# Performance work log

Hardware: AMD Instinct MI355X
Metric: run time of the kernel (lower is better)

The kernel has to match this reference:

```python
import jax, jax.numpy as jnp
import numpy as np

# physics constants (from initBatteryParams)
R_GAS = 8.3144621
F = 96487.0
ALPHA = 0.5
VOL = 2.2e-5
VOLS = 0.1 * VOL
VOLB = VOL - VOLS
SN = 2e-4
SP = 2e-4
KN = 2e4
KP = 2e4
TO = 10.0
TSN = 90.0
TSP = 90.0
U0P = 4.03
U0N = 0.01
QMAX_BASE = 10000.0
RO_BASE = 10.0
DT = 1.0

B = 2097152


def setup_inputs() -> dict:
    key = jax.random.key(0)
    ks = jax.random.split(key, 10)
    f32 = jnp.float32
    # per-batch learned params (qMax ~ 14000/10000, Ro ~ 0.15/10)
    qMax = jnp.full((B,), 1.4, dtype=f32)
    Ro = jnp.full((B,), 0.015, dtype=f32)
    tDiffusion = jnp.asarray(7e6, dtype=f32)
    # physically plausible initial state (get_initial_state): Tb=292.1, V's ~0,
    # qnB~qnBMax=7560, qnS~qnSMax=840, qpB~qpBMin=5040, qpS~qpSMin=560
    n = lambda k, s: jax.random.normal(k, s, dtype=f32)
    Tb = jnp.full((B,), 292.1, dtype=f32)
    Vo = 0.01 * n(ks[0], (B,))
    Vsn = 0.01 * n(ks[1], (B,))
    Vsp = 0.01 * n(ks[2], (B,))
    qnB = 7560.0 * (1.0 + 0.01 * n(ks[3], (B,)))
    qnS = 840.0 * (1.0 + 0.01 * n(ks[4], (B,)))
    qpB = 5040.0 * (1.0 + 0.01 * n(ks[5], (B,)))
    qpS = 560.0 * (1.0 + 0.01 * n(ks[6], (B,)))
    states = jnp.stack([Tb, Vo, Vsn, Vsp, qnB, qnS, qpB, qpS], axis=1)
    # applied current ~ [1, 3) A
    inputs = 1.0 + 2.0 * jax.random.uniform(ks[7], (B, 1), dtype=f32)
    # MLPp: Dense(1->8 tanh) -> Dense(8->4 tanh) -> Dense(4->1); MLPn: Dense(1->1)
    wk = jax.random.split(ks[8], 4)
    Wp1 = 0.5 * n(wk[0], (1, 8)); bp1 = jnp.zeros((8,), f32)
    Wp2 = 0.5 * n(wk[1], (8, 4)); bp2 = jnp.zeros((4,), f32)
    Wp3 = 0.5 * n(wk[2], (4, 1)); bp3 = jnp.zeros((1,), f32)
    Wn = jnp.full((1, 1), 0.0016, dtype=f32)  # MLPn fit to map [0,1]->[-8e-4,8e-4]
    bn = jnp.full((1,), -0.0008, dtype=f32)
    return dict(inputs=inputs, states=states, qMax=qMax, Ro=Ro,
                tDiffusion=tDiffusion, Wp1=Wp1, bp1=bp1, Wp2=Wp2, bp2=bp2,
                Wp3=Wp3, bp3=bp3, Wn=Wn, bn=bn)


def _battery_step(inputs, states, qMax, Ro, tDiffusion,
                  Wp1, bp1, Wp2, bp2, Wp3, bp3, Wn, bn):
    Tb, Vo, Vsn, Vsp, qnB, qnS, qpB, qpS = [states[:, k] for k in range(8)]
    i = inputs[:, 0]
    qSMax = qMax * QMAX_BASE * VOLS / VOL  # [B]

    # ---- getNextState ----
    xpS = jnp.clip(qpS / qSMax, 1e-18, 1.0)
    xnS = jnp.clip(qnS / qSMax, 1e-18, 1.0)
    Jn0 = 1e-18 + KN * (1.0 - xnS) ** ALPHA * xnS ** ALPHA
    Jp0 = 1e-18 + KP * (1.0 - xpS) ** ALPHA * xpS ** ALPHA
    qdotDiffBSn = (qnB / VOLB - qnS / VOLS) / tDiffusion
    qdotDiffBSp = (qpB / VOLB - qpS / VOLS) / tDiffusion
    Vodot = (i * Ro * RO_BASE - Vo) / TO
    VsnNom = R_GAS * Tb / F / ALPHA * jnp.arcsinh((i / SN) / (2.0 * Jn0))
    VspNom = R_GAS * Tb / F / ALPHA * jnp.arcsinh((i / SP) / (2.0 * Jp0))
    Vsndot = (VsnNom - Vsn) / TSN
    Vspdot = (VspNom - Vsp) / TSP
    Xnew = jnp.stack([
        Tb,                               # Tbdot = 0
        Vo + Vodot * DT,
        Vsn + Vsndot * DT,
        Vsp + Vspdot * DT,
        qnB - qdotDiffBSn * DT,
        qnS + (qdotDiffBSn - i) * DT,
        qpB - qdotDiffBSp * DT,
        qpS + (i + qdotDiffBSp) * DT,
    ], axis=1)  # [B,8]

    # ---- getNextOutput (on Xnew) ----
    Tb2, Vo2, Vsn2, Vsp2 = Xnew[:, 0], Xnew[:, 1], Xnew[:, 2], Xnew[:, 3]
    xpS2 = Xnew[:, 7] / qSMax  # no clip here, matching original
    xnS2 = Xnew[:, 5] / qSMax
    h = jnp.tanh(xpS2[:, None] @ Wp1 + bp1)
    h = jnp.tanh(h @ Wp2 + bp2)
    VepMLP = (h @ Wp3 + bp3)[:, 0]
    VenMLP = (xnS2[:, None] @ Wn + bn)[:, 0]
    safe_log_p = jnp.clip((1.0 - xpS2) / xpS2, 1e-18, 1e18)
    safe_log_n = jnp.clip((1.0 - xnS2) / xnS2, 1e-18, 1e18)
    Vep = U0P + R_GAS * Tb2 / F * jnp.log(safe_log_p) + VepMLP
    Ven = U0N + R_GAS * Tb2 / F * jnp.log(safe_log_n) + VenMLP
    V = Vep - Ven - Vo2 - Vsn2 - Vsp2
    return V[:, None], Xnew


def reference(inputs, states, qMax, Ro, tDiffusion,
              Wp1, bp1, Wp2, bp2, Wp3, bp3, Wn, bn):
    return _battery_step(inputs, states, qMax, Ro, tDiffusion,
                         Wp1, bp1, Wp2, bp2, Wp3, bp3, Wn, bn)
```

## Files before the change

kernel.cpp:

```cpp
#include <hip/hip_runtime.h>

#define DEVFN __device__ __forceinline__

DEVFN float fast_rcp(float x) { return __builtin_amdgcn_rcpf(x); }

DEVFN float fast_tanh(float x) {
    float e = __expf(2.0f * x);
    return 1.0f - 2.0f * fast_rcp(e + 1.0f);
}

DEVFN float fast_asinh(float z) {
    float az = fabsf(z);
    float r = __logf(az + sqrtf(fmaf(az, az, 1.0f)));
    return copysignf(r, z);
}

constexpr int ELEMS = 4;

DEVFN void battery_compute(
    float4 s0, float4 s1, float i, float qm, float ro, float invTD,
    const float* __restrict__ Wp1, const float* __restrict__ bp1,
    const float* __restrict__ Wp2, const float* __restrict__ bp2,
    const float* __restrict__ Wp3, const float* __restrict__ bp3,
    const float* __restrict__ Wn,  const float* __restrict__ bn,
    float& V, float4& o0, float4& o1)
{
    const float invVOLB = 1.0f / 1.98e-5f;
    const float invVOLS = 1.0f / 2.2e-6f;
    const float RTFA    = 8.3144621f / 96487.0f / 0.5f;
    const float RF      = 8.3144621f / 96487.0f;

    const float Tb = s0.x, Vo = s0.y, Vsn = s0.z, Vsp = s0.w;
    const float qnB = s1.x, qnS = s1.y, qpB = s1.z, qpS = s1.w;

    const float qSMax = qm * 1000.0f;
    const float rq    = fast_rcp(qSMax);

    float xpS = fminf(fmaxf(qpS * rq, 1e-18f), 1.0f);
    float xnS = fminf(fmaxf(qnS * rq, 1e-18f), 1.0f);

    float Jn0 = 1e-18f + 20000.0f * sqrtf((1.0f - xnS) * xnS);
    float Jp0 = 1e-18f + 20000.0f * sqrtf((1.0f - xpS) * xpS);

    float qdotn = (qnB * invVOLB - qnS * invVOLS) * invTD;
    float qdotp = (qpB * invVOLB - qpS * invVOLS) * invTD;

    float Vodot = (i * ro * 10.0f - Vo) * 0.1f;

    float zn = i * 2500.0f * fast_rcp(Jn0);
    float zp = i * 2500.0f * fast_rcp(Jp0);
    float VsnNom = RTFA * Tb * fast_asinh(zn);
    float VspNom = RTFA * Tb * fast_asinh(zp);

    const float X0 = Tb;
    const float X1 = Vo + Vodot;
    const float X2 = Vsn + (VsnNom - Vsn) * (1.0f / 90.0f);
    const float X3 = Vsp + (VspNom - Vsp) * (1.0f / 90.0f);
    const float X4 = qnB - qdotn;
    const float X5 = qnS + (qdotn - i);
    const float X6 = qpB - qdotp;
    const float X7 = qpS + (i + qdotp);

    const float xp2 = X7 * rq;
    const float xn2 = X5 * rq;

    float h1[8];
#pragma unroll
    for (int j = 0; j < 8; ++j)
        h1[j] = fast_tanh(fmaf(xp2, Wp1[j], bp1[j]));

    float h2[4];
#pragma unroll
    for (int k = 0; k < 4; ++k) {
        float acc = bp2[k];
#pragma unroll
        for (int j = 0; j < 8; ++j)
            acc = fmaf(h1[j], Wp2[j * 4 + k], acc);
        h2[k] = fast_tanh(acc);
    }

    float VepMLP = bp3[0];
#pragma unroll
    for (int k = 0; k < 4; ++k)
        VepMLP = fmaf(h2[k], Wp3[k], VepMLP);

    const float VenMLP = fmaf(xn2, Wn[0], bn[0]);

    float ratio = ((1.0f - xp2) * xn2) * fast_rcp(xp2 * (1.0f - xn2));
    float logr  = __logf(ratio);

    V = (4.03f - 0.01f) + RF * X0 * logr + VepMLP - VenMLP - X1 - X2 - X3;
    o0 = make_float4(X0, X1, X2, X3);
    o1 = make_float4(X4, X5, X6, X7);
}

template<bool EXACT>
__global__ __launch_bounds__(256) void battery_step_kernel(
    const float* __restrict__ inputs, const float* __restrict__ states,
    const float* __restrict__ qMax, const float* __restrict__ Ro,
    const float* __restrict__ tDiff,
    const float* __restrict__ Wp1, const float* __restrict__ bp1,
    const float* __restrict__ Wp2, const float* __restrict__ bp2,
    const float* __restrict__ Wp3, const float* __restrict__ bp3,
    const float* __restrict__ Wn,  const float* __restrict__ bn,
    float* __restrict__ outV, float* __restrict__ outX, int n)
{
    const int t      = blockIdx.x * 256 + threadIdx.x;
    const int stride = gridDim.x * 256;

    const float invTD = fast_rcp(tDiff[0]);

    int idx = t;
    float4 s0, s1; float cur, qm, ro;
    bool ok = EXACT || (idx < n);
    if (ok) {
        s0  = ((const float4*)states)[idx * 2 + 0];
        s1  = ((const float4*)states)[idx * 2 + 1];
        cur = inputs[idx];
        qm  = qMax[idx];
        ro  = Ro[idx];
    }

#pragma unroll
    for (int e = 0; e < ELEMS; ++e) {
        float4 ns0, ns1; float ncur, nqm, nro;
        bool nok = false;
        if (e + 1 < ELEMS) {
            int nidx = idx + stride;
            nok = EXACT || (nidx < n);
            if (nok) {
                ns0  = ((const float4*)states)[nidx * 2 + 0];
                ns1  = ((const float4*)states)[nidx * 2 + 1];
                ncur = inputs[nidx];
                nqm  = qMax[nidx];
                nro  = Ro[nidx];
            }
        }

        if (ok) {
            float V; float4 o0, o1;
            battery_compute(s0, s1, cur, qm, ro, invTD,
                            Wp1, bp1, Wp2, bp2, Wp3, bp3, Wn, bn,
                            V, o0, o1);
            outV[idx] = V;
            ((float4*)outX)[idx * 2 + 0] = o0;
            ((float4*)outX)[idx * 2 + 1] = o1;
        }

        idx += stride;
        s0 = ns0; s1 = ns1; cur = ncur; qm = nqm; ro = nro; ok = nok;
    }
}

__global__ __launch_bounds__(256) void stream_probe_kernel(
    const float* __restrict__ inputs, const float* __restrict__ states,
    const float* __restrict__ qMax, const float* __restrict__ Ro,
    float* __restrict__ wsOut)
{
    const int t      = blockIdx.x * 256 + threadIdx.x;
    const int stride = gridDim.x * 256;
    float acc = 0.0f;
#pragma unroll
    for (int e = 0; e < ELEMS; ++e) {
        int idx = t + e * stride;
        float4 s0 = ((const float4*)states)[idx * 2 + 0];
        float4 s1 = ((const float4*)states)[idx * 2 + 1];
        acc += s0.x + s0.y + s0.z + s0.w + s1.x + s1.y + s1.z + s1.w
             + inputs[idx] + qMax[idx] + Ro[idx];
        wsOut[idx] = acc;
    }
}

extern "C" void kernel_launch(void* const* d_in, const int* in_sizes, int n_in,
                              void* d_out, int out_size, void* d_ws, size_t ws_size,
                              hipStream_t stream) {
    const float* inputs = (const float*)d_in[0];
    const float* states = (const float*)d_in[1];
    const float* qMax   = (const float*)d_in[2];
    const float* Ro     = (const float*)d_in[3];
    const float* tDiff  = (const float*)d_in[4];
    const float* Wp1    = (const float*)d_in[5];
    const float* bp1    = (const float*)d_in[6];
    const float* Wp2    = (const float*)d_in[7];
    const float* bp2    = (const float*)d_in[8];
    const float* Wp3    = (const float*)d_in[9];
    const float* bp3    = (const float*)d_in[10];
    const float* Wn     = (const float*)d_in[11];
    const float* bn     = (const float*)d_in[12];

    const int n = in_sizes[0];
    float* outV = (float*)d_out;
    float* outX = (float*)d_out + n;

    const int threads = 256;
    const int chunk   = threads * ELEMS;

    if (n % chunk == 0) {
        const int blocks = n / chunk;
        battery_step_kernel<true><<<dim3(blocks), dim3(threads), 0, stream>>>(
            inputs, states, qMax, Ro, tDiff,
            Wp1, bp1, Wp2, bp2, Wp3, bp3, Wn, bn, outV, outX, n);
        if (ws_size >= (size_t)n * sizeof(float)) {
            stream_probe_kernel<<<dim3(blocks), dim3(threads), 0, stream>>>(
                inputs, states, qMax, Ro, (float*)d_ws);
        }
    } else {
        const int blocks = (n + chunk - 1) / chunk;
        battery_step_kernel<false><<<dim3(blocks), dim3(threads), 0, stream>>>(
            inputs, states, qMax, Ro, tDiff,
            Wp1, bp1, Wp2, bp2, Wp3, bp3, Wn, bn, outV, outX, n);
    }
}
```

Baseline: 188.4 us.

## Drop probe kernel, batch all loads upfront, use rsqrt and nontemporal stores

Removes the extra streaming probe kernel that re-read the inputs after the main step kernel, eliminating a redundant memory pass. The main kernel now processes 8 elements per thread and issues all loads before computing, and writes outputs with nontemporal stores. The Jn0/Jp0 reciprocal-of-sqrt path is replaced by a single rsqrt with the tiny additive epsilon dropped, and launch bounds request 4 waves of occupancy. Holding more loaded data in registers may raise register pressure.

```diff
diff --git a/kernel.cpp b/kernel.cpp
--- a/kernel.cpp
+++ b/kernel.cpp
@@ -2,7 +2,10 @@
 
 #define DEVFN __device__ __forceinline__
 
-DEVFN float fast_rcp(float x) { return __builtin_amdgcn_rcpf(x); }
+typedef float f32x4 __attribute__((ext_vector_type(4)));
+
+DEVFN float fast_rcp(float x)   { return __builtin_amdgcn_rcpf(x); }
+DEVFN float fast_rsqrt(float x) { return __builtin_amdgcn_rsqf(x); }
 
 DEVFN float fast_tanh(float x) {
     float e = __expf(2.0f * x);
@@ -15,15 +18,15 @@
     return copysignf(r, z);
 }
 
-constexpr int ELEMS = 4;
+constexpr int ELEMS = 8;
 
 DEVFN void battery_compute(
-    float4 s0, float4 s1, float i, float qm, float ro, float invTD,
+    f32x4 s0, f32x4 s1, float i, float qm, float ro, float invTD,
     const float* __restrict__ Wp1, const float* __restrict__ bp1,
     const float* __restrict__ Wp2, const float* __restrict__ bp2,
     const float* __restrict__ Wp3, const float* __restrict__ bp3,
     const float* __restrict__ Wn,  const float* __restrict__ bn,
-    float& V, float4& o0, float4& o1)
+    float& V, f32x4& o0, f32x4& o1)
 {
     const float invVOLB = 1.0f / 1.98e-5f;
     const float invVOLS = 1.0f / 2.2e-6f;
@@ -39,16 +42,16 @@
     float xpS = fminf(fmaxf(qpS * rq, 1e-18f), 1.0f);
     float xnS = fminf(fmaxf(qnS * rq, 1e-18f), 1.0f);
 
-    float Jn0 = 1e-18f + 20000.0f * sqrtf((1.0f - xnS) * xnS);
-    float Jp0 = 1e-18f + 20000.0f * sqrtf((1.0f - xpS) * xpS);
+    float un = (1.0f - xnS) * xnS;
+    float up = (1.0f - xpS) * xpS;
+    float zn = i * 0.125f * fast_rsqrt(fmaxf(un, 1e-30f));
+    float zp = i * 0.125f * fast_rsqrt(fmaxf(up, 1e-30f));
 
     float qdotn = (qnB * invVOLB - qnS * invVOLS) * invTD;
     float qdotp = (qpB * invVOLB - qpS * invVOLS) * invTD;
 
     float Vodot = (i * ro * 10.0f - Vo) * 0.1f;
 
-    float zn = i * 2500.0f * fast_rcp(Jn0);
-    float zp = i * 2500.0f * fast_rcp(Jp0);
     float VsnNom = RTFA * Tb * fast_asinh(zn);
     float VspNom = RTFA * Tb * fast_asinh(zp);
 
@@ -90,12 +93,12 @@
     float logr  = __logf(ratio);
 
     V = (4.03f - 0.01f) + RF * X0 * logr + VepMLP - VenMLP - X1 - X2 - X3;
-    o0 = make_float4(X0, X1, X2, X3);
-    o1 = make_float4(X4, X5, X6, X7);
+    o0.x = X0; o0.y = X1; o0.z = X2; o0.w = X3;
+    o1.x = X4; o1.y = X5; o1.z = X6; o1.w = X7;
 }
 
 template<bool EXACT>
-__global__ __launch_bounds__(256) void battery_step_kernel(
+__global__ __launch_bounds__(256, 4) void battery_step_kernel(
     const float* __restrict__ inputs, const float* __restrict__ states,
     const float* __restrict__ qMax, const float* __restrict__ Ro,
     const float* __restrict__ tDiff,
@@ -110,64 +113,33 @@
 
     const float invTD = fast_rcp(tDiff[0]);
 
-    int idx = t;
-    float4 s0, s1; float cur, qm, ro;
-    bool ok = EXACT || (idx < n);
-    if (ok) {
-        s0  = ((const float4*)states)[idx * 2 + 0];
-        s1  = ((const float4*)states)[idx * 2 + 1];
-        cur = inputs[idx];
-        qm  = qMax[idx];
-        ro  = Ro[idx];
+    f32x4 s0[ELEMS], s1[ELEMS];
+    float cur[ELEMS], qm[ELEMS], ro[ELEMS];
+    bool  ok[ELEMS];
+#pragma unroll
+    for (int e = 0; e < ELEMS; ++e) {
+        const int idx = t + e * stride;
+        ok[e] = EXACT || (idx < n);
+        if (ok[e]) {
+            s0[e]  = ((const f32x4*)states)[idx * 2 + 0];
+            s1[e]  = ((const f32x4*)states)[idx * 2 + 1];
+            cur[e] = inputs[idx];
+            qm[e]  = qMax[idx];
+            ro[e]  = Ro[idx];
+        }
     }
 
 #pragma unroll
     for (int e = 0; e < ELEMS; ++e) {
-        float4 ns0, ns1; float ncur, nqm, nro;
-        bool nok = false;
-        if (e + 1 < ELEMS) {
-            int nidx = idx + stride;
-            nok = EXACT || (nidx < n);
-            if (nok) {
-                ns0  = ((const float4*)states)[nidx * 2 + 0];
-                ns1  = ((const float4*)states)[nidx * 2 + 1];
-                ncur = inputs[nidx];
-                nqm  = qMax[nidx];
-                nro  = Ro[nidx];
-            }
-        }
-
-        if (ok) {
-            float V; float4 o0, o1;
-            battery_compute(s0, s1, cur, qm, ro, invTD,
-                            Wp1, bp1, Wp2, bp2, Wp3, bp3, Wn, bn,
-                            V, o0, o1);
-            outV[idx] = V;
-            ((float4*)outX)[idx * 2 + 0] = o0;
-            ((float4*)outX)[idx * 2 + 1] = o1;
-        }
-
-        idx += stride;
-        s0 = ns0; s1 = ns1; cur = ncur; qm = nqm; ro = nro; ok = nok;
-    }
-}
-
-__global__ __launch_bounds__(256) void stream_probe_kernel(
-    const float* __restrict__ inputs, const float* __restrict__ states,
-    const float* __restrict__ qMax, const float* __restrict__ Ro,
-    float* __restrict__ wsOut)
-{
-    const int t      = blockIdx.x * 256 + threadIdx.x;
-    const int stride = gridDim.x * 256;
-    float acc = 0.0f;
-#pragma unroll
-    for (int e = 0; e < ELEMS; ++e) {
-        int idx = t + e * stride;
-        float4 s0 = ((const float4*)states)[idx * 2 + 0];
-        float4 s1 = ((const float4*)states)[idx * 2 + 1];
-        acc += s0.x + s0.y + s0.z + s0.w + s1.x + s1.y + s1.z + s1.w
-             + inputs[idx] + qMax[idx] + Ro[idx];
-        wsOut[idx] = acc;
+        if (!ok[e]) continue;
+        const int idx = t + e * stride;
+        float V; f32x4 o0, o1;
+        battery_compute(s0[e], s1[e], cur[e], qm[e], ro[e], invTD,
+                        Wp1, bp1, Wp2, bp2, Wp3, bp3, Wn, bn,
+                        V, o0, o1);
+        __builtin_nontemporal_store(V, outV + idx);
+        __builtin_nontemporal_store(o0, (f32x4*)outX + idx * 2 + 0);
+        __builtin_nontemporal_store(o1, (f32x4*)outX + idx * 2 + 1);
     }
 }
 
@@ -200,10 +172,6 @@
         battery_step_kernel<true><<<dim3(blocks), dim3(threads), 0, stream>>>(
             inputs, states, qMax, Ro, tDiff,
             Wp1, bp1, Wp2, bp2, Wp3, bp3, Wn, bn, outV, outX, n);
-        if (ws_size >= (size_t)n * sizeof(float)) {
-            stream_probe_kernel<<<dim3(blocks), dim3(threads), 0, stream>>>(
-                inputs, states, qMax, Ro, (float*)d_ws);
-        }
     } else {
         const int blocks = (n + chunk - 1) / chunk;
         battery_step_kernel<false><<<dim3(blocks), dim3(threads), 0, stream>>>(
```

Result: slower. 198.9 us (+5.6%).
